# Optimization experiments

Hardware: AMD Instinct MI355X
Metric: run time of the kernel (lower is better)

## Reference

```python
import jax, jax.numpy as jnp
import numpy as np

B = 128
T = 784
H = 256
N_CLASSES = 10


def setup_inputs() -> dict:
    key = jax.random.key(0)
    ks = jax.random.split(key, 7)
    s = 1.0 / np.sqrt(H)
    inputs = jax.random.normal(ks[0], (B, T), dtype=jnp.float32)
    # fixed permutation, matching np.random.RandomState(92916).permutation(784)
    perm = jnp.asarray(np.random.RandomState(92916).permutation(T), dtype=jnp.int32)
    W_ih = jax.random.uniform(ks[1], (4 * H, 1), jnp.float32, -s, s)
    W_hh = jax.random.uniform(ks[2], (4 * H, H), jnp.float32, -s, s)
    b_ih = jax.random.uniform(ks[3], (4 * H,), jnp.float32, -s, s)
    b_hh = jax.random.uniform(ks[4], (4 * H,), jnp.float32, -s, s)
    lin_W = jax.random.uniform(ks[5], (N_CLASSES, H), jnp.float32, -s, s)
    lin_b = jax.random.uniform(ks[6], (N_CLASSES,), jnp.float32, -s, s)
    return {"inputs": inputs, "perm": perm, "W_ih": W_ih, "W_hh": W_hh,
            "b_ih": b_ih, "b_hh": b_hh, "lin_W": lin_W, "lin_b": lin_b}


def reference(inputs, perm, W_ih, W_hh, b_ih, b_hh, lin_W, lin_b):
    # permuted sequential MNIST
    x = inputs[:, perm]                      # [B, T]
    b = b_ih + b_hh                          # [4H]
    w_in = W_ih[:, 0]                        # [4H], input size is 1

    def step(carry, x_t):
        h, c = carry                         # each [B, H]
        gates = x_t[:, None] * w_in[None, :] + h @ W_hh.T + b  # [B, 4H]
        i, f, g, o = jnp.split(gates, 4, axis=-1)
        i = jax.nn.sigmoid(i)
        f = jax.nn.sigmoid(f)
        g = jnp.tanh(g)
        o = jax.nn.sigmoid(o)
        c = f * c + i * g
        h = o * jnp.tanh(c)
        return (h, c), None

    h0 = jnp.zeros((x.shape[0], W_hh.shape[1]), dtype=x.dtype)
    (h, c), _ = jax.lax.scan(step, (h0, h0), x.T)  # scan over T, xs [T, B]
    return h @ lin_W.T + lin_b               # [B, n_classes]
```

## Files before the change

### kernel.cpp

```cpp
#include <hip/hip_runtime.h>

#define TSTEPS 784
#define BATCH  128
#define HID    256
#define WPG    8
#define BG     4
#define NGRP   (BATCH / BG)
#define COLS   32
#define RLOC   128
#define MAXFAST 256
typedef unsigned long long u64;

__global__ void prep_x(const float* __restrict__ in, const int* __restrict__ perm,
                       float* __restrict__ xp) {
    int b = blockIdx.x;
    for (int t = threadIdx.x; t < TSTEPS; t += blockDim.x)
        xp[b * TSTEPS + t] = in[b * TSTEPS + perm[t]];
}

__global__ void prep_slots(u64* __restrict__ slots) {
    int i = blockIdx.x * blockDim.x + threadIdx.x;
    if (i < BATCH * HID)          slots[i] = 0ull;
    else if (i < 2 * BATCH * HID) slots[i] = 0xFFFFFFFF00000000ull;
}

__global__ __launch_bounds__(1024, 4) void lstm_kernel(
    const float* __restrict__ Whh, const float* __restrict__ Wih,
    const float* __restrict__ bih, const float* __restrict__ bhh,
    const float* __restrict__ xp, u64* __restrict__ slots)
{
    __shared__ float h_lds[BG * HID];
    __shared__ float gate_lds[BG * 132];
    __shared__ float x_lds[BG * TSTEPS];
    __shared__ float c_lds[BG * COLS];
    __shared__ float bias_lds[RLOC];
    __shared__ float win_lds[RLOC];

    const int tid = threadIdx.x;
    const int g       = blockIdx.x & 31;
    const int wgi     = blockIdx.x >> 5;
    const int B0      = g * BG;
    const int colbase = wgi * COLS;

    const int r = tid >> 3;
    const int s = tid & 7;
    const int gate = r >> 5;
    const int R = gate * 256 + colbase + (r & 31);

    float4 w0, w1, w2, w3, w4, w5, w6, w7;
    {
        const float4* wp = (const float4*)(Whh + R * HID + s * 32);
        w0 = wp[(0 + s) & 7]; w1 = wp[(1 + s) & 7];
        w2 = wp[(2 + s) & 7]; w3 = wp[(3 + s) & 7];
        w4 = wp[(4 + s) & 7]; w5 = wp[(5 + s) & 7];
        w6 = wp[(6 + s) & 7]; w7 = wp[(7 + s) & 7];
    }
    #define KEEP4(V) asm volatile("" : "+v"((V).x), "+v"((V).y), "+v"((V).z), "+v"((V).w))
    KEEP4(w0); KEEP4(w1); KEEP4(w2); KEEP4(w3);
    KEEP4(w4); KEEP4(w5); KEEP4(w6); KEEP4(w7);
    #undef KEEP4

    if (tid < RLOC) {
        int gr = (tid >> 5) * 256 + colbase + (tid & 31);
        bias_lds[tid] = bih[gr] + bhh[gr];
        win_lds[tid]  = Wih[gr];
    }
    #pragma unroll
    for (int b = 0; b < BG; ++b)
        if (tid < TSTEPS) x_lds[b * TSTEPS + tid] = xp[(B0 + b) * TSTEPS + tid];
    if (tid < BG * COLS) c_lds[tid] = 0.f;
    __syncthreads();

    const int pb = tid >> 8, pk = tid & 255;
    u64* const slot0 = slots + (B0 + pb) * HID + pk;
    u64* const slot1 = slots + BATCH * HID + (B0 + pb) * HID + pk;

    bool fast_ok = true;

    for (int t = 0; t < TSTEPS; ++t) {
        {
            u64* sp = (t & 1) ? slot1 : slot0;
            u64 v = 0;
            if (fast_ok) {
                int it = 0;
                for (;;) {
                    asm volatile("global_load_dwordx2 %0, %1, off sc0\n\t"
                                 "s_waitcnt vmcnt(0)"
                                 : "=v"(v) : "v"(sp) : "memory");
                    if ((unsigned)(v >> 32) == (unsigned)t) break;
                    if (++it >= MAXFAST) { fast_ok = false; break; }
                }
            }
            if (!fast_ok) {
                do {
                    v = __hip_atomic_load(sp, __ATOMIC_RELAXED, __HIP_MEMORY_SCOPE_AGENT);
                } while ((unsigned)(v >> 32) != (unsigned)t);
            }
            h_lds[tid] = __uint_as_float((unsigned)v);
        }
        __syncthreads();

        float a0 = 0.f, a1 = 0.f, a2 = 0.f, a3 = 0.f;
        const float* hbase = h_lds + s * 32;
        #define DOT_STEP(d, wd)                                              \
        {                                                                    \
            int off = (((d) + s) & 7) * 4;                                   \
            float4 hq0 = *(const float4*)(hbase + off);                      \
            float4 hq1 = *(const float4*)(hbase + 256 + off);                \
            float4 hq2 = *(const float4*)(hbase + 512 + off);                \
            float4 hq3 = *(const float4*)(hbase + 768 + off);                \
            a0 = fmaf(wd.x, hq0.x, a0); a0 = fmaf(wd.y, hq0.y, a0);          \
            a0 = fmaf(wd.z, hq0.z, a0); a0 = fmaf(wd.w, hq0.w, a0);          \
            a1 = fmaf(wd.x, hq1.x, a1); a1 = fmaf(wd.y, hq1.y, a1);          \
            a1 = fmaf(wd.z, hq1.z, a1); a1 = fmaf(wd.w, hq1.w, a1);          \
            a2 = fmaf(wd.x, hq2.x, a2); a2 = fmaf(wd.y, hq2.y, a2);          \
            a2 = fmaf(wd.z, hq2.z, a2); a2 = fmaf(wd.w, hq2.w, a2);          \
            a3 = fmaf(wd.x, hq3.x, a3); a3 = fmaf(wd.y, hq3.y, a3);          \
            a3 = fmaf(wd.w, hq3.w, a3); a3 = fmaf(wd.z, hq3.z, a3);          \
        }
        DOT_STEP(0, w0) DOT_STEP(1, w1) DOT_STEP(2, w2) DOT_STEP(3, w3)
        DOT_STEP(4, w4) DOT_STEP(5, w5) DOT_STEP(6, w6) DOT_STEP(7, w7)
        #undef DOT_STEP

        #pragma unroll
        for (int m = 1; m < 8; m <<= 1) {
            a0 += __shfl_xor(a0, m, 64);
            a1 += __shfl_xor(a1, m, 64);
            a2 += __shfl_xor(a2, m, 64);
            a3 += __shfl_xor(a3, m, 64);
        }
        if (s < BG) {
            float sum = (s == 0) ? a0 : (s == 1) ? a1 : (s == 2) ? a2 : a3;
            float xv = x_lds[s * TSTEPS + t];
            float full = fmaf(win_lds[r], xv, sum + bias_lds[r]);
            float act;
            if (gate == 2) act = 2.f / (1.f + __expf(-2.f * full)) - 1.f;
            else           act = 1.f / (1.f + __expf(-full));
            gate_lds[s * 132 + r] = act;
        }
        __syncthreads();

        if (tid < BG * COLS) {
            int b = tid >> 5, j = tid & 31;
            float iv = gate_lds[b * 132 + j];
            float fv = gate_lds[b * 132 + 32 + j];
            float gv = gate_lds[b * 132 + 64 + j];
            float ov = gate_lds[b * 132 + 96 + j];
            float cn = fmaf(fv, c_lds[tid], iv * gv);
            c_lds[tid] = cn;
            float tc = 2.f / (1.f + __expf(-2.f * cn)) - 1.f;
            float hn = ov * tc;
            u64 val = ((u64)(unsigned)(t + 1) << 32) | (u64)__float_as_uint(hn);
            u64* dp = slots + ((t + 1) & 1) * (BATCH * HID)
                            + (B0 + b) * HID + colbase + j;
            asm volatile("global_store_dwordx2 %0, %1, off sc0"
                         :: "v"(dp), "v"(val) : "memory");
            __hip_atomic_store(dp, val, __ATOMIC_RELAXED, __HIP_MEMORY_SCOPE_AGENT);
        }
    }
}

__global__ void out_kernel(const u64* __restrict__ slots, const float* __restrict__ linW,
                           const float* __restrict__ linb, float* __restrict__ out) {
    __shared__ float hl[HID];
    int b = blockIdx.x;
    for (int k = threadIdx.x; k < HID; k += blockDim.x)
        hl[k] = __uint_as_float((unsigned)slots[b * HID + k]);
    __syncthreads();
    if (threadIdx.x < 10) {
        int n = threadIdx.x;
        float acc = linb[n];
        for (int k = 0; k < HID; ++k) acc = fmaf(hl[k], linW[n * HID + k], acc);
        out[b * 10 + n] = acc;
    }
}

extern "C" void kernel_launch(void* const* d_in, const int* in_sizes, int n_in,
                              void* d_out, int out_size, void* d_ws, size_t ws_size,
                              hipStream_t stream) {
    const float* inputs = (const float*)d_in[0];
    const int*   perm   = (const int*)d_in[1];
    const float* Wih    = (const float*)d_in[2];
    const float* Whh    = (const float*)d_in[3];
    const float* bih    = (const float*)d_in[4];
    const float* bhh    = (const float*)d_in[5];
    const float* linW   = (const float*)d_in[6];
    const float* linb   = (const float*)d_in[7];
    float* out = (float*)d_out;

    u64*   slots = (u64*)d_ws;
    float* xp    = (float*)(slots + 2 * BATCH * HID);

    prep_x<<<BATCH, 256, 0, stream>>>(inputs, perm, xp);
    prep_slots<<<(2 * BATCH * HID + 255) / 256, 256, 0, stream>>>(slots);
    lstm_kernel<<<NGRP * WPG, 1024, 0, stream>>>(Whh, Wih, bih, bhh, xp, slots);
    out_kernel<<<BATCH, 64, 0, stream>>>(slots, linW, linb, out);
}
```

Baseline: 2.473 ms.

## Poll only remote hidden slices with wide loads, keep local slice in LDS

The cross-block exchange of the hidden state is reworked. Only 448 threads now poll, and each reads two slots with a 16-byte load that bypasses caches (sc0 sc1). The block's own 32 columns are written straight into a double-buffered LDS copy of h, so they are never polled from global memory. The step-zero poll is skipped because h starts at zero, the redundant non-atomic store is dropped, and the dot product uses packed v_pk_fma_f32. The aim is to cut polling traffic and latency on the per-step critical path, at the cost of a different accumulation order and more complex slot-validity checks.

Measured after the change: 2.346 ms. -5.1%, faster.

```diff
diff --git a/kernel.cpp b/kernel.cpp
--- a/kernel.cpp
+++ b/kernel.cpp
@@ -8,8 +8,12 @@
 #define NGRP   (BATCH / BG)
 #define COLS   32
 #define RLOC   128
-#define MAXFAST 256
+#define NPOLL  448
+#define MAXFAST 512
 typedef unsigned long long u64;
+typedef float v4f __attribute__((ext_vector_type(4)));
+typedef float v2f __attribute__((ext_vector_type(2)));
+typedef unsigned int v4u __attribute__((ext_vector_type(4)));
 
 __global__ void prep_x(const float* __restrict__ in, const int* __restrict__ perm,
                        float* __restrict__ xp) {
@@ -24,12 +28,15 @@
     else if (i < 2 * BATCH * HID) slots[i] = 0xFFFFFFFF00000000ull;
 }
 
+#define PK_FMA(acc, a, b) \
+    asm("v_pk_fma_f32 %0, %1, %2, %0" : "+v"(acc) : "v"(a), "v"(b))
+
 __global__ __launch_bounds__(1024, 4) void lstm_kernel(
     const float* __restrict__ Whh, const float* __restrict__ Wih,
     const float* __restrict__ bih, const float* __restrict__ bhh,
     const float* __restrict__ xp, u64* __restrict__ slots)
 {
-    __shared__ float h_lds[BG * HID];
+    __shared__ float h_lds[2][BG * HID];
     __shared__ float gate_lds[BG * 132];
     __shared__ float x_lds[BG * TSTEPS];
     __shared__ float c_lds[BG * COLS];
@@ -47,18 +54,18 @@
     const int gate = r >> 5;
     const int R = gate * 256 + colbase + (r & 31);
 
-    float4 w0, w1, w2, w3, w4, w5, w6, w7;
+    v4f w0, w1, w2, w3, w4, w5, w6, w7;
     {
-        const float4* wp = (const float4*)(Whh + R * HID + s * 32);
+        const v4f* wp = (const v4f*)(Whh + R * HID + s * 32);
         w0 = wp[(0 + s) & 7]; w1 = wp[(1 + s) & 7];
         w2 = wp[(2 + s) & 7]; w3 = wp[(3 + s) & 7];
         w4 = wp[(4 + s) & 7]; w5 = wp[(5 + s) & 7];
         w6 = wp[(6 + s) & 7]; w7 = wp[(7 + s) & 7];
     }
-    #define KEEP4(V) asm volatile("" : "+v"((V).x), "+v"((V).y), "+v"((V).z), "+v"((V).w))
-    KEEP4(w0); KEEP4(w1); KEEP4(w2); KEEP4(w3);
-    KEEP4(w4); KEEP4(w5); KEEP4(w6); KEEP4(w7);
-    #undef KEEP4
+    #define KEEPV(V) asm volatile("" : "+v"(V))
+    KEEPV(w0); KEEPV(w1); KEEPV(w2); KEEPV(w3);
+    KEEPV(w4); KEEPV(w5); KEEPV(w6); KEEPV(w7);
+    #undef KEEPV
 
     if (tid < RLOC) {
         int gr = (tid >> 5) * 256 + colbase + (tid & 31);
@@ -69,58 +76,80 @@
     for (int b = 0; b < BG; ++b)
         if (tid < TSTEPS) x_lds[b * TSTEPS + tid] = xp[(B0 + b) * TSTEPS + tid];
     if (tid < BG * COLS) c_lds[tid] = 0.f;
+    h_lds[0][tid] = 0.f;
+
+    int pb_ = 0, uu_ = 0;
+    u64* ppair0 = slots;
+    u64* ppair1 = slots;
+    if (tid < NPOLL) {
+        int b = tid / 112, u = tid - 112 * b;
+        int uu = u + (u >= (colbase >> 1) ? 16 : 0);
+        pb_ = b; uu_ = uu;
+        ppair0 = slots + (B0 + b) * HID + 2 * uu;
+        ppair1 = slots + BATCH * HID + (B0 + b) * HID + 2 * uu;
+    }
+    bool fast_ok = true;
     __syncthreads();
 
-    const int pb = tid >> 8, pk = tid & 255;
-    u64* const slot0 = slots + (B0 + pb) * HID + pk;
-    u64* const slot1 = slots + BATCH * HID + (B0 + pb) * HID + pk;
-
-    bool fast_ok = true;
-
     for (int t = 0; t < TSTEPS; ++t) {
-        {
-            u64* sp = (t & 1) ? slot1 : slot0;
-            u64 v = 0;
+        const int cur = t & 1;
+        if (t > 0 && tid < NPOLL) {
+            u64* sp = cur ? ppair1 : ppair0;
+            const unsigned tt = (unsigned)t;
+            v4u v;
             if (fast_ok) {
                 int it = 0;
                 for (;;) {
-                    asm volatile("global_load_dwordx2 %0, %1, off sc0\n\t"
+                    asm volatile("global_load_dwordx4 %0, %1, off sc0 sc1\n\t"
                                  "s_waitcnt vmcnt(0)"
                                  : "=v"(v) : "v"(sp) : "memory");
-                    if ((unsigned)(v >> 32) == (unsigned)t) break;
+                    if (v.y == tt && v.w == tt) break;
                     if (++it >= MAXFAST) { fast_ok = false; break; }
                 }
             }
             if (!fast_ok) {
-                do {
-                    v = __hip_atomic_load(sp, __ATOMIC_RELAXED, __HIP_MEMORY_SCOPE_AGENT);
-                } while ((unsigned)(v >> 32) != (unsigned)t);
+                u64 a, b2;
+                do { a = __hip_atomic_load(sp, __ATOMIC_RELAXED, __HIP_MEMORY_SCOPE_AGENT);
+                } while ((unsigned)(a >> 32) != tt);
+                do { b2 = __hip_atomic_load(sp + 1, __ATOMIC_RELAXED, __HIP_MEMORY_SCOPE_AGENT);
+                } while ((unsigned)(b2 >> 32) != tt);
+                v.x = (unsigned)a; v.z = (unsigned)b2;
             }
-            h_lds[tid] = __uint_as_float((unsigned)v);
+            float2 hv;
+            hv.x = __uint_as_float(v.x);
+            hv.y = __uint_as_float(v.z);
+            *(float2*)&h_lds[cur][pb_ * HID + 2 * uu_] = hv;
         }
         __syncthreads();
 
-        float a0 = 0.f, a1 = 0.f, a2 = 0.f, a3 = 0.f;
-        const float* hbase = h_lds + s * 32;
-        #define DOT_STEP(d, wd)                                              \
-        {                                                                    \
-            int off = (((d) + s) & 7) * 4;                                   \
-            float4 hq0 = *(const float4*)(hbase + off);                      \
-            float4 hq1 = *(const float4*)(hbase + 256 + off);                \
-            float4 hq2 = *(const float4*)(hbase + 512 + off);                \
-            float4 hq3 = *(const float4*)(hbase + 768 + off);                \
-            a0 = fmaf(wd.x, hq0.x, a0); a0 = fmaf(wd.y, hq0.y, a0);          \
-            a0 = fmaf(wd.z, hq0.z, a0); a0 = fmaf(wd.w, hq0.w, a0);          \
-            a1 = fmaf(wd.x, hq1.x, a1); a1 = fmaf(wd.y, hq1.y, a1);          \
-            a1 = fmaf(wd.z, hq1.z, a1); a1 = fmaf(wd.w, hq1.w, a1);          \
-            a2 = fmaf(wd.x, hq2.x, a2); a2 = fmaf(wd.y, hq2.y, a2);          \
-            a2 = fmaf(wd.z, hq2.z, a2); a2 = fmaf(wd.w, hq2.w, a2);          \
-            a3 = fmaf(wd.x, hq3.x, a3); a3 = fmaf(wd.y, hq3.y, a3);          \
-            a3 = fmaf(wd.w, hq3.w, a3); a3 = fmaf(wd.z, hq3.z, a3);          \
+        v2f acc0 = {0.f, 0.f}, acc1 = {0.f, 0.f}, acc2 = {0.f, 0.f}, acc3 = {0.f, 0.f};
+        const float* hbase = h_lds[cur] + s * 32;
+        #define DOT_STEP(d, wd)                                               \
+        {                                                                     \
+            int off = (((d) + s) & 7) * 4;                                    \
+            v4f hq0 = *(const v4f*)(hbase + off);                             \
+            v4f hq1 = *(const v4f*)(hbase + 256 + off);                       \
+            v4f hq2 = *(const v4f*)(hbase + 512 + off);                       \
+            v4f hq3 = *(const v4f*)(hbase + 768 + off);                       \
+            v2f wlo = __builtin_shufflevector(wd, wd, 0, 1);                  \
+            v2f whi = __builtin_shufflevector(wd, wd, 2, 3);                  \
+            PK_FMA(acc0, wlo, __builtin_shufflevector(hq0, hq0, 0, 1));       \
+            PK_FMA(acc0, whi, __builtin_shufflevector(hq0, hq0, 2, 3));       \
+            PK_FMA(acc1, wlo, __builtin_shufflevector(hq1, hq1, 0, 1));       \
+            PK_FMA(acc1, whi, __builtin_shufflevector(hq1, hq1, 2, 3));       \
+            PK_FMA(acc2, wlo, __builtin_shufflevector(hq2, hq2, 0, 1));       \
+            PK_FMA(acc2, whi, __builtin_shufflevector(hq2, hq2, 2, 3));       \
+            PK_FMA(acc3, wlo, __builtin_shufflevector(hq3, hq3, 0, 1));       \
+            PK_FMA(acc3, whi, __builtin_shufflevector(hq3, hq3, 2, 3));       \
         }
         DOT_STEP(0, w0) DOT_STEP(1, w1) DOT_STEP(2, w2) DOT_STEP(3, w3)
         DOT_STEP(4, w4) DOT_STEP(5, w5) DOT_STEP(6, w6) DOT_STEP(7, w7)
         #undef DOT_STEP
+
+        float a0 = acc0.x + acc0.y;
+        float a1 = acc1.x + acc1.y;
+        float a2 = acc2.x + acc2.y;
+        float a3 = acc3.x + acc3.y;
 
         #pragma unroll
         for (int m = 1; m < 8; m <<= 1) {
@@ -133,9 +162,9 @@
             float sum = (s == 0) ? a0 : (s == 1) ? a1 : (s == 2) ? a2 : a3;
             float xv = x_lds[s * TSTEPS + t];
             float full = fmaf(win_lds[r], xv, sum + bias_lds[r]);
-            float act;
-            if (gate == 2) act = 2.f / (1.f + __expf(-2.f * full)) - 1.f;
-            else           act = 1.f / (1.f + __expf(-full));
+            float pre = (gate == 2) ? 2.f * full : full;
+            float rec = 1.f / (1.f + __expf(-pre));
+            float act = (gate == 2) ? fmaf(2.f, rec, -1.f) : rec;
             gate_lds[s * 132 + r] = act;
         }
         __syncthreads();
@@ -150,11 +179,10 @@
             c_lds[tid] = cn;
             float tc = 2.f / (1.f + __expf(-2.f * cn)) - 1.f;
             float hn = ov * tc;
+            h_lds[cur ^ 1][b * HID + colbase + j] = hn;
             u64 val = ((u64)(unsigned)(t + 1) << 32) | (u64)__float_as_uint(hn);
             u64* dp = slots + ((t + 1) & 1) * (BATCH * HID)
                             + (B0 + b) * HID + colbase + j;
-            asm volatile("global_store_dwordx2 %0, %1, off sc0"
-                         :: "v"(dp), "v"(val) : "memory");
             __hip_atomic_store(dp, val, __ATOMIC_RELAXED, __HIP_MEMORY_SCOPE_AGENT);
         }
     }
```
